# Kernel tuning notes

Hardware: AMD Instinct MI355X
Metric: run time of the kernel (lower is better)

Reference implementation:

```python
import jax, jax.numpy as jnp
import numpy as np

EPS = 1e-6

def safe_softmax(x, axis=-1):
    x_max = jnp.max(x, axis=axis, keepdims=True)
    x_exp = jnp.exp(x - x_max)
    return x_exp / (jnp.sum(x_exp, axis=axis, keepdims=True) + EPS)

def setup_inputs() -> dict:
    key = jax.random.key(0)
    ks = jax.random.split(key, 8)
    B, S, D = 16, 2048, 1024
    scale = 1.0 / np.sqrt(D)
    x = jax.random.normal(ks[0], (B, S, D), dtype=jnp.float32)
    y = jax.random.normal(ks[1], (B, S, D), dtype=jnp.float32)
    Wq = jax.random.normal(ks[2], (D, D), dtype=jnp.float32) * scale
    bq = jnp.zeros((D,), dtype=jnp.float32)
    Wk = jax.random.normal(ks[3], (D, D), dtype=jnp.float32) * scale
    bk = jnp.zeros((D,), dtype=jnp.float32)
    Wv = jax.random.normal(ks[4], (D, D), dtype=jnp.float32) * scale
    bv = jnp.zeros((D,), dtype=jnp.float32)
    return {"x": x, "y": y, "Wq": Wq, "bq": bq, "Wk": Wk, "bk": bk, "Wv": Wv, "bv": bv}

def reference(x, y, Wq, bq, Wk, bk, Wv, bv):
    # Q/K/V projections: [B, S, D]
    Q = jnp.einsum('bsd,df->bsf', x, Wq) + bq
    K = jnp.einsum('bsd,df->bsf', y, Wk) + bk
    V = jnp.einsum('bsd,df->bsf', y, Wv) + bv
    D = K.shape[-1]
    # single-head attention over full [B, Sq, Skv] score matrix
    logits = jnp.einsum('bqd,bkd->bqk', Q, K) / jnp.sqrt(jnp.float32(D))
    attn = safe_softmax(logits, axis=-1)
    out = jnp.einsum('bqk,bkd->bqd', attn, V)
    return out + x
```

## Files before the change

kernel.cpp:

```cpp
#include <hip/hip_runtime.h>
#include <hip/hip_bf16.h>

typedef __attribute__((ext_vector_type(8))) short bf16x8;
typedef __attribute__((ext_vector_type(4))) float f32x4;

__device__ __forceinline__ float bf2f(short u) {
  union { unsigned int u; float f; } c;
  c.u = ((unsigned int)(unsigned short)u) << 16;
  return c.f;
}
__device__ __forceinline__ short f2bf(float f) {
  union { float f; unsigned int u; } c; c.f = f;
  unsigned int r = (c.u + 0x7fffu + ((c.u >> 16) & 1u)) >> 16;
  return (short)(unsigned short)r;
}

__device__ __forceinline__ void gload16(const void* g, void* l) {
  __builtin_amdgcn_global_load_lds(
      (const __attribute__((address_space(1))) unsigned int*)g,
      (__attribute__((address_space(3))) unsigned int*)l, 16, 0, 0);
}

__global__ __launch_bounds__(256) void cvt_k(const float* __restrict__ in,
                                             short* __restrict__ out, int n4) {
  int i = blockIdx.x * blockDim.x + threadIdx.x;
  const int stride = gridDim.x * blockDim.x;
  for (; i < n4; i += stride) {
    float4 v = ((const float4*)in)[i];
    short4 o;
    o.x = f2bf(v.x); o.y = f2bf(v.y); o.z = f2bf(v.z); o.w = f2bf(v.w);
    ((short4*)out)[i] = o;
  }
}

__global__ __launch_bounds__(256) void cvtT_k(const float* __restrict__ W,
                                              short* __restrict__ Wt) {
  __shared__ float tile[32][33];
  const int n0 = blockIdx.x * 32, k0 = blockIdx.y * 32;
  const int tr = threadIdx.x >> 5;
  const int tc = threadIdx.x & 31;
#pragma unroll
  for (int p = 0; p < 4; ++p)
    tile[p * 8 + tr][tc] = W[(long long)(k0 + p * 8 + tr) * 1024 + n0 + tc];
  __syncthreads();
#pragma unroll
  for (int p = 0; p < 4; ++p)
    Wt[(long long)(n0 + p * 8 + tr) * 1024 + k0 + tc] = f2bf(tile[tc][p * 8 + tr]);
}


#define STG6(sp, ld8, dOff) do { \
  gload16((sp), Ls + (dOff)); \
  gload16((const char*)(sp) + (ld8), Ls + (dOff) + 512); } while (0)

#define RD_A6(BUF, QM) do { \
  _Pragma("unroll") \
  for (int mi = 0; mi < 4; ++mi) { \
    aR[mi][0] = *(const bf16x8*)(Ls + (BUF) + (QM)*8192 + arow + mi*1024 + aO0); \
    aR[mi][1] = *(const bf16x8*)(Ls + (BUF) + (QM)*8192 + arow + mi*1024 + aO1); \
  } } while (0)

#define RD_B6(DST, BUF, QN) do { \
  _Pragma("unroll") \
  for (int ni = 0; ni < 2; ++ni) { \
    DST[ni][0] = *(const bf16x8*)(Ls + (BUF) + 16384 + (QN)*8192 + brow + ni*1024 + aO0); \
    DST[ni][1] = *(const bf16x8*)(Ls + (BUF) + 16384 + (QN)*8192 + brow + ni*1024 + aO1); \
  } } while (0)

#define SYNCIN6 do { \
  __builtin_amdgcn_sched_barrier(0); \
  __builtin_amdgcn_s_barrier(); \
  asm volatile("s_waitcnt lgkmcnt(0)" ::: "memory"); \
  __builtin_amdgcn_sched_barrier(0); \
  __builtin_amdgcn_s_setprio(1); } while (0)

#define SYNCOUT6 do { \
  __builtin_amdgcn_s_setprio(0); \
  __builtin_amdgcn_s_barrier(); } while (0)

#define MF166(ACCQ, BB) do { \
  _Pragma("unroll") \
  for (int mi = 0; mi < 4; ++mi) { \
    _Pragma("unroll") \
    for (int ni = 0; ni < 2; ++ni) { \
      ACCQ[mi][ni] = __builtin_amdgcn_mfma_f32_16x16x32_bf16(aR[mi][0], BB[ni][0], ACCQ[mi][ni], 0, 0, 0); \
      ACCQ[mi][ni] = __builtin_amdgcn_mfma_f32_16x16x32_bf16(aR[mi][1], BB[ni][1], ACCQ[mi][ni], 0, 0, 0); \
    } \
  } } while (0)

template<int EPI>
__global__ __launch_bounds__(512) void gemm256_k(
    const short* __restrict__ A, const short* __restrict__ Bt,
    void* __restrict__ Cv, const float* __restrict__ X,
    int K, int lda, int ldb, int ldc) {
  __shared__ __align__(16) short Ls[65536];

  const int lane = threadIdx.x & 63;
  const int w = threadIdx.x >> 6;
  const int wm = w >> 2, wn = w & 3;
  const int w1k = w * 1024;
  const int l15 = lane & 15;
  const int g4 = lane >> 4;
  const int p8 = lane & 7;
  const int r8 = lane >> 3;
  const int aO0 = (g4 ^ p8) << 3;
  const int aO1 = ((4 + g4) ^ p8) << 3;
  const int arow = (wm * 64 + l15) * 64;
  const int brow = (wn * 32 + l15) * 64;

  const int gx = gridDim.x, gy = gridDim.y;
  const int nwg = gx * gy * gridDim.z;
  int lid = blockIdx.x + gx * (blockIdx.y + gy * blockIdx.z);
  lid = (lid & 7) * (nwg >> 3) + (lid >> 3);
  const int bx = lid % gx;
  const int rem = lid / gx;
  const int by = rem % gy;

  const int n0 = bx * 256;
  const int m0 = by * 256;
  const int nt = K >> 6;
  const int nit = nt >> 1;

  const long long ldaB = 2LL * lda, ldbB = 2LL * ldb;
  const long long ldaB8 = 8 * ldaB, ldbB8 = 8 * ldbB;
  const long long hOffA = 128 * ldaB, hOffB = 128 * ldbB;

  const char* pA = (const char*)A
      + (long long)(m0 + w * 16 + r8) * ldaB + ((p8 ^ r8) << 4);
  const char* pB = (const char*)Bt
      + (long long)(n0 + w * 16 + r8) * ldbB + ((p8 ^ r8) << 4);

  f32x4 acc[2][2][4][2] = {};
  bf16x8 aR[4][2], bR0[2][2], bR1[2][2];

  STG6(pA,                 ldaB8, 0 + w1k);
  STG6(pA + hOffA,         ldaB8, 8192 + w1k);
  STG6(pB,                 ldbB8, 16384 + w1k);
  STG6(pB + hOffB,         ldbB8, 24576 + w1k);
  STG6(pA + 128,           ldaB8, 32768 + w1k);
  STG6(pA + 128 + hOffA,   ldaB8, 40960 + w1k);
  STG6(pB + 128,           ldbB8, 49152 + w1k);
  STG6(pB + 128 + hOffB,   ldbB8, 57344 + w1k);
  asm volatile("s_waitcnt vmcnt(8)" ::: "memory");
  __builtin_amdgcn_s_barrier();

  for (int j = 0; j < nit; ++j) {
    const bool st = (j + 1 < nit);

    RD_A6(0, 0); RD_B6(bR0, 0, 0);
    SYNCIN6; MF166(acc[0][0], bR0); SYNCOUT6;
    RD_B6(bR1, 0, 1);
    if (st) { STG6(pA + 256, ldaB8, 0 + w1k);
              STG6(pB + 256, ldbB8, 16384 + w1k); }
    SYNCIN6; MF166(acc[0][1], bR1); SYNCOUT6;
    RD_A6(0, 1);
    if (st) STG6(pB + 256 + hOffB, ldbB8, 24576 + w1k);
    SYNCIN6; MF166(acc[1][1], bR1); SYNCOUT6;
    if (st) STG6(pA + 256 + hOffA, ldaB8, 8192 + w1k);
    SYNCIN6; MF166(acc[1][0], bR0);
    __builtin_amdgcn_s_setprio(0);
    if (st) asm volatile("s_waitcnt vmcnt(8)" ::: "memory");
    else    asm volatile("s_waitcnt vmcnt(0)" ::: "memory");
    __builtin_amdgcn_s_barrier();

    RD_A6(32768, 0); RD_B6(bR0, 32768, 0);
    SYNCIN6; MF166(acc[0][0], bR0); SYNCOUT6;
    RD_B6(bR1, 32768, 1);
    if (st) { STG6(pA + 384, ldaB8, 32768 + w1k);
              STG6(pB + 384, ldbB8, 49152 + w1k); }
    SYNCIN6; MF166(acc[0][1], bR1); SYNCOUT6;
    RD_A6(32768, 1);
    if (st) STG6(pB + 384 + hOffB, ldbB8, 57344 + w1k);
    SYNCIN6; MF166(acc[1][1], bR1); SYNCOUT6;
    if (st) STG6(pA + 384 + hOffA, ldaB8, 40960 + w1k);
    SYNCIN6; MF166(acc[1][0], bR0);
    __builtin_amdgcn_s_setprio(0);
    if (st) asm volatile("s_waitcnt vmcnt(8)" ::: "memory");
    __builtin_amdgcn_s_barrier();

    pA += 256; pB += 256;
  }

  const int rB = g4 * 4;
  if (EPI == 0) {
    short* C = (short*)Cv;
#pragma unroll
    for (int qn = 0; qn < 2; ++qn)
#pragma unroll
      for (int ni = 0; ni < 2; ++ni) {
        const int col = n0 + qn * 128 + wn * 32 + ni * 16 + l15;
        const float bv = X[col];
#pragma unroll
        for (int qm = 0; qm < 2; ++qm)
#pragma unroll
          for (int mi = 0; mi < 4; ++mi)
#pragma unroll
            for (int r = 0; r < 4; ++r) {
              const int row = m0 + qm * 128 + wm * 64 + mi * 16 + rB + r;
              C[(long long)row * ldc + col] = f2bf(acc[qm][qn][mi][ni][r] + bv);
            }
      }
  } else {
    short* C = (short*)Cv;
#pragma unroll
    for (int qn = 0; qn < 2; ++qn)
#pragma unroll
      for (int ni = 0; ni < 2; ++ni) {
        const int col = n0 + qn * 128 + wn * 32 + ni * 16 + l15;
        const int b2 = col >> 11;
        const int s = col & 2047;
#pragma unroll
        for (int qm = 0; qm < 2; ++qm)
#pragma unroll
          for (int mi = 0; mi < 4; ++mi)
#pragma unroll
            for (int r = 0; r < 4; ++r) {
              const int row = m0 + qm * 128 + wm * 64 + mi * 16 + rB + r;
              C[(long long)b2 * 2097152 + (long long)row * 2048 + s] =
                  f2bf(acc[qm][qn][mi][ni][r] + X[row]);
            }
      }
  }
}


template<int EPI>
__global__ __launch_bounds__(512, 4) void gemm8_k(
    const short* __restrict__ A, const short* __restrict__ Bt,
    void* __restrict__ Cv, const float* __restrict__ X,
    int K, int lda, int ldb, int ldc,
    long long strA, long long strB, long long strC, long long strX, float scale) {
  __shared__ __align__(16) short Ls[36864];

  const int lane = threadIdx.x & 63;
  const int w = threadIdx.x >> 6;
  const int wm = w >> 1, wn = w & 1;
  const int l15 = lane & 15;
  const int g4 = lane >> 4;
  const int swR = ((g4 ^ ((l15 >> 1) & 3)) << 3);
  const int arow = (wm * 64 + l15) * 32 + swR;
  const int brow = (wn * 64 + l15) * 32 + swR;
  const int sg = (lane & 3) ^ ((lane >> 3) & 3);

  const int gx = gridDim.x, gy = gridDim.y;
  const int nwg = gx * gy * gridDim.z;
  int lid = blockIdx.x + gx * (blockIdx.y + gy * blockIdx.z);
  lid = (lid & 7) * (nwg >> 3) + (lid >> 3);
  const int bx = lid % gx;
  const int rem = lid / gx;
  const int by = rem % gy;
  const int bz = rem / gy;

  const int n0 = bx * 128;
  const int m0 = by * 256;
  const int nt = K >> 5;

  const long long ldaB = 2LL * lda, ldbB = 2LL * ldb;
  const long long ldaB16 = 16 * ldaB;

  const char* pA = (const char*)(A + (long long)bz * strA)
      + (long long)(m0 + w * 32 + (lane >> 2)) * ldaB + sg * 16;
  const char* pB = (const char*)(Bt + (long long)bz * strB)
      + (long long)(n0 + w * 16 + (lane >> 2)) * ldbB + sg * 16;

  short* dA = Ls + w * 1024;
  short* dB = Ls + 8192 + w * 512;

  f32x4 acc[4][4] = {};

#pragma unroll
  for (int i = 0; i < 3; ++i) {
    const char* qA = pA + i * 64;
    gload16(qA,           dA + i * 12288);
    gload16(qA + ldaB16,  dA + i * 12288 + 512);
    gload16(pB + i * 64,  dB + i * 12288);
  }
  asm volatile("s_waitcnt vmcnt(6)" ::: "memory");
  __builtin_amdgcn_s_barrier();

  int cur = 0;
  for (int t = 0; t < nt; ++t) {
    const int bufO = cur * 12288;
    bf16x8 aR[4], bR[4];
#pragma unroll
    for (int mi = 0; mi < 4; ++mi)
      aR[mi] = *(const bf16x8*)(Ls + bufO + arow + mi * 512);
#pragma unroll
    for (int ni = 0; ni < 4; ++ni)
      bR[ni] = *(const bf16x8*)(Ls + bufO + 8192 + brow + ni * 512);
    asm volatile("s_waitcnt lgkmcnt(0)" ::: "memory");
    __builtin_amdgcn_s_barrier();
    if (t + 3 < nt) {
      const char* qA = pA + (t + 3) * 64;
      gload16(qA,          dA + bufO);
      gload16(qA + ldaB16, dA + bufO + 512);
      gload16(pB + (t + 3) * 64, dB + bufO);
    }
    __builtin_amdgcn_sched_barrier(0);
    __builtin_amdgcn_s_setprio(1);
#pragma unroll
    for (int mi = 0; mi < 4; ++mi)
#pragma unroll
      for (int ni = 0; ni < 4; ++ni)
        acc[mi][ni] = __builtin_amdgcn_mfma_f32_16x16x32_bf16(
            aR[mi], bR[ni], acc[mi][ni], 0, 0, 0);
    __builtin_amdgcn_s_setprio(0);
    if (t + 3 < nt)      asm volatile("s_waitcnt vmcnt(6)" ::: "memory");
    else if (t + 2 < nt) asm volatile("s_waitcnt vmcnt(3)" ::: "memory");
    else                 asm volatile("s_waitcnt vmcnt(0)" ::: "memory");
    __builtin_amdgcn_s_barrier();
    cur = (cur == 2) ? 0 : cur + 1;
  }

  const int rB = g4 * 4;
  if (EPI == 1) {
    short* C = (short*)Cv + (long long)bz * strC;
#pragma unroll
    for (int ni = 0; ni < 4; ++ni) {
      const int col = n0 + wn * 64 + ni * 16 + l15;
#pragma unroll
      for (int mi = 0; mi < 4; ++mi)
#pragma unroll
        for (int r = 0; r < 4; ++r) {
          const int row = m0 + wm * 64 + mi * 16 + rB + r;
          C[(long long)row * ldc + col] = f2bf(acc[mi][ni][r] * scale);
        }
    }
  } else {
    float* C = (float*)Cv + (long long)bz * strC;
    const float* Xb = X + (long long)bz * strX;
#pragma unroll
    for (int ni = 0; ni < 4; ++ni) {
      const int col = n0 + wn * 64 + ni * 16 + l15;
#pragma unroll
      for (int mi = 0; mi < 4; ++mi)
#pragma unroll
        for (int r = 0; r < 4; ++r) {
          const int row = m0 + wm * 64 + mi * 16 + rB + r;
          const long long idx = (long long)row * ldc + col;
          C[idx] = acc[mi][ni][r] + Xb[idx];
        }
    }
  }
}

__global__ __launch_bounds__(256) void softmax_k(short* __restrict__ P) {
  __shared__ float redm[4];
  __shared__ float reds[4];
  const long long row = blockIdx.x;
  short* p = P + row * 2048;
  const int t = threadIdx.x;
  const int w = t >> 6, lane = t & 63;
  bf16x8 v = *(const bf16x8*)(p + t * 8);
  float f[8];
  float mx = -3.0e38f;
#pragma unroll
  for (int j = 0; j < 8; ++j) { f[j] = bf2f(v[j]); mx = fmaxf(mx, f[j]); }
#pragma unroll
  for (int o = 32; o > 0; o >>= 1) mx = fmaxf(mx, __shfl_xor(mx, o));
  if (lane == 0) redm[w] = mx;
  __syncthreads();
  mx = fmaxf(fmaxf(redm[0], redm[1]), fmaxf(redm[2], redm[3]));
  float s = 0.f;
#pragma unroll
  for (int j = 0; j < 8; ++j) { f[j] = __expf(f[j] - mx); s += f[j]; }
#pragma unroll
  for (int o = 32; o > 0; o >>= 1) s += __shfl_xor(s, o);
  if (lane == 0) reds[w] = s;
  __syncthreads();
  s = reds[0] + reds[1] + reds[2] + reds[3];
  const float inv = 1.0f / (s + 1e-6f);
  bf16x8 o8;
#pragma unroll
  for (int j = 0; j < 8; ++j) o8[j] = f2bf(f[j] * inv);
  *(bf16x8*)(p + t * 8) = o8;
}

extern "C" void kernel_launch(void* const* d_in, const int* in_sizes, int n_in,
                              void* d_out, int out_size, void* d_ws, size_t ws_size,
                              hipStream_t stream) {
  const float* x  = (const float*)d_in[0];
  const float* y  = (const float*)d_in[1];
  const float* Wq = (const float*)d_in[2];
  const float* bq = (const float*)d_in[3];
  const float* Wk = (const float*)d_in[4];
  const float* bk = (const float*)d_in[5];
  const float* Wv = (const float*)d_in[6];
  const float* bv = (const float*)d_in[7];
  float* out = (float*)d_out;

  const long long SD  = 2048LL * 1024;
  const long long BSD = 16LL * SD;
  const long long SS  = 2048LL * 2048;

  char* ws = (char*)d_ws;
  short* xb  = (short*)ws;
  short* yb  = xb + BSD;
  short* Sl  = (short*)ws;
  short* Qb  = (short*)(ws + 134217728);
  short* Kb  = Qb + BSD;
  short* Vt  = Kb + BSD;
  short* Wqt = Vt + BSD;
  short* Wkt = Wqt + 1024 * 1024;
  short* Wvt = Wkt + 1024 * 1024;

  cvt_k<<<2048, 256, 0, stream>>>(x, xb, (int)(BSD / 4));
  cvt_k<<<2048, 256, 0, stream>>>(y, yb, (int)(BSD / 4));

  cvtT_k<<<dim3(32, 32), 256, 0, stream>>>(Wq, Wqt);
  cvtT_k<<<dim3(32, 32), 256, 0, stream>>>(Wk, Wkt);
  cvtT_k<<<dim3(32, 32), 256, 0, stream>>>(Wv, Wvt);

  gemm256_k<0><<<dim3(4, 128, 1), 512, 0, stream>>>(
      xb, Wqt, Qb, bq, 1024, 1024, 1024, 1024);
  gemm256_k<0><<<dim3(4, 128, 1), 512, 0, stream>>>(
      yb, Wkt, Kb, bk, 1024, 1024, 1024, 1024);
  gemm256_k<3><<<dim3(128, 4, 1), 512, 0, stream>>>(
      Wvt, yb, Vt, bv, 1024, 1024, 1024, 0);

  gemm8_k<1><<<dim3(16, 8, 16), 512, 0, stream>>>(
      Qb, Kb, Sl, nullptr, 1024, 1024, 1024, 2048, SD, SD, SS, 0, 0.03125f);

  softmax_k<<<32768, 256, 0, stream>>>(Sl);

  gemm8_k<2><<<dim3(8, 8, 16), 512, 0, stream>>>(
      Sl, Vt, out, x, 2048, 2048, 2048, 1024, SS, SD, SD, SD, 1.f);

  (void)in_sizes; (void)n_in; (void)out_size; (void)ws_size;
}
```

Before: 739.3 us.

## Compute P·V in FP8 with scaled softmax output and permuted K-layout

The softmax now writes probabilities scaled by 256 as FP8 into a separate buffer, and the V projection epilogue stores V^T as FP8. Both use a permuted position ordering so that each lane's 16-byte LDS read feeds two fp8 16x16x32 MFMAs. A new pv8_k kernel runs the P·V GEMM with fp8 MFMAs, then unscales and adds the residual. This halves the bytes moved for P and V and uses the faster fp8 MFMA rate, at the cost of lower precision in the attention weights and V.

```diff
diff --git a/kernel.cpp b/kernel.cpp
--- a/kernel.cpp
+++ b/kernel.cpp
@@ -3,6 +3,7 @@
 
 typedef __attribute__((ext_vector_type(8))) short bf16x8;
 typedef __attribute__((ext_vector_type(4))) float f32x4;
+typedef __attribute__((ext_vector_type(2))) long i64x2;
 
 __device__ __forceinline__ float bf2f(short u) {
   union { unsigned int u; float f; } c;
@@ -19,6 +20,10 @@
   __builtin_amdgcn_global_load_lds(
       (const __attribute__((address_space(1))) unsigned int*)g,
       (__attribute__((address_space(3))) unsigned int*)l, 16, 0, 0);
+}
+
+__device__ __forceinline__ int fp8_g(int s) {
+  return (s >> 6) * 64 + ((s >> 3) & 3) * 16 + ((s >> 5) & 1) * 8 + (s & 7);
 }
 
 __global__ __launch_bounds__(256) void cvt_k(const float* __restrict__ in,
@@ -201,7 +206,7 @@
             }
       }
   } else {
-    short* C = (short*)Cv;
+    unsigned char* C = (unsigned char*)Cv;
 #pragma unroll
     for (int qn = 0; qn < 2; ++qn)
 #pragma unroll
@@ -209,6 +214,7 @@
         const int col = n0 + qn * 128 + wn * 32 + ni * 16 + l15;
         const int b2 = col >> 11;
         const int s = col & 2047;
+        const int gs = fp8_g(s);
 #pragma unroll
         for (int qm = 0; qm < 2; ++qm)
 #pragma unroll
@@ -216,8 +222,10 @@
 #pragma unroll
             for (int r = 0; r < 4; ++r) {
               const int row = m0 + qm * 128 + wm * 64 + mi * 16 + rB + r;
-              C[(long long)b2 * 2097152 + (long long)row * 2048 + s] =
-                  f2bf(acc[qm][qn][mi][ni][r] + X[row]);
+              const float v = acc[qm][qn][mi][ni][r] + X[row];
+              const unsigned d = __builtin_amdgcn_cvt_pk_fp8_f32(v, v, 0, false);
+              C[(long long)b2 * 2097152 + (long long)row * 2048 + gs] =
+                  (unsigned char)(d & 0xff);
             }
       }
   }
@@ -313,42 +321,27 @@
   }
 
   const int rB = g4 * 4;
-  if (EPI == 1) {
-    short* C = (short*)Cv + (long long)bz * strC;
-#pragma unroll
-    for (int ni = 0; ni < 4; ++ni) {
-      const int col = n0 + wn * 64 + ni * 16 + l15;
-#pragma unroll
-      for (int mi = 0; mi < 4; ++mi)
-#pragma unroll
-        for (int r = 0; r < 4; ++r) {
-          const int row = m0 + wm * 64 + mi * 16 + rB + r;
-          C[(long long)row * ldc + col] = f2bf(acc[mi][ni][r] * scale);
-        }
-    }
-  } else {
-    float* C = (float*)Cv + (long long)bz * strC;
-    const float* Xb = X + (long long)bz * strX;
-#pragma unroll
-    for (int ni = 0; ni < 4; ++ni) {
-      const int col = n0 + wn * 64 + ni * 16 + l15;
-#pragma unroll
-      for (int mi = 0; mi < 4; ++mi)
-#pragma unroll
-        for (int r = 0; r < 4; ++r) {
-          const int row = m0 + wm * 64 + mi * 16 + rB + r;
-          const long long idx = (long long)row * ldc + col;
-          C[idx] = acc[mi][ni][r] + Xb[idx];
-        }
-    }
-  }
-}
-
-__global__ __launch_bounds__(256) void softmax_k(short* __restrict__ P) {
+  short* C = (short*)Cv + (long long)bz * strC;
+#pragma unroll
+  for (int ni = 0; ni < 4; ++ni) {
+    const int col = n0 + wn * 64 + ni * 16 + l15;
+#pragma unroll
+    for (int mi = 0; mi < 4; ++mi)
+#pragma unroll
+      for (int r = 0; r < 4; ++r) {
+        const int row = m0 + wm * 64 + mi * 16 + rB + r;
+        C[(long long)row * ldc + col] = f2bf(acc[mi][ni][r] * scale);
+      }
+  }
+  (void)X; (void)strX;
+}
+
+__global__ __launch_bounds__(256) void softmax8_k(const short* __restrict__ Sl,
+                                                  unsigned char* __restrict__ P8) {
   __shared__ float redm[4];
   __shared__ float reds[4];
   const long long row = blockIdx.x;
-  short* p = P + row * 2048;
+  const short* p = Sl + row * 2048;
   const int t = threadIdx.x;
   const int w = t >> 6, lane = t & 63;
   bf16x8 v = *(const bf16x8*)(p + t * 8);
@@ -369,11 +362,116 @@
   if (lane == 0) reds[w] = s;
   __syncthreads();
   s = reds[0] + reds[1] + reds[2] + reds[3];
-  const float inv = 1.0f / (s + 1e-6f);
-  bf16x8 o8;
-#pragma unroll
-  for (int j = 0; j < 8; ++j) o8[j] = f2bf(f[j] * inv);
-  *(bf16x8*)(p + t * 8) = o8;
+  const float inv = 256.0f / (s + 1e-6f);
+  unsigned d0 = __builtin_amdgcn_cvt_pk_fp8_f32(f[0] * inv, f[1] * inv, 0, false);
+  d0 = __builtin_amdgcn_cvt_pk_fp8_f32(f[2] * inv, f[3] * inv, d0, true);
+  unsigned d1 = __builtin_amdgcn_cvt_pk_fp8_f32(f[4] * inv, f[5] * inv, 0, false);
+  d1 = __builtin_amdgcn_cvt_pk_fp8_f32(f[6] * inv, f[7] * inv, d1, true);
+  const int grp = t >> 3, pc = t & 7;
+  unsigned char* dst = P8 + row * 2048 + grp * 64 + (pc & 3) * 16 + (pc >> 2) * 8;
+  *(unsigned long long*)dst =
+      (unsigned long long)d0 | ((unsigned long long)d1 << 32);
+}
+
+
+__global__ __launch_bounds__(512, 4) void pv8_k(
+    const unsigned char* __restrict__ P8, const unsigned char* __restrict__ V8,
+    float* __restrict__ Out, const float* __restrict__ x) {
+  __shared__ __align__(16) char Ls[73728];
+
+  const int lane = threadIdx.x & 63;
+  const int w = threadIdx.x >> 6;
+  const int wm = w >> 1, wn = w & 1;
+  const int l15 = lane & 15;
+  const int g4 = lane >> 4;
+  const int swB = ((g4 ^ ((l15 >> 1) & 3)) << 4);
+  const int arow = (wm * 64 + l15) * 64 + swB;
+  const int brow = (wn * 64 + l15) * 64 + swB;
+  const int sg = (lane & 3) ^ ((lane >> 3) & 3);
+
+  const int nwg = 1024;
+  int lid = blockIdx.x + 8 * (blockIdx.y + 8 * blockIdx.z);
+  lid = (lid & 7) * (nwg >> 3) + (lid >> 3);
+  const int bx = lid % 8;
+  const int rem = lid / 8;
+  const int by = rem % 8;
+  const int bz = rem / 8;
+  const int n0 = bx * 128, m0 = by * 256;
+  const int nt = 32;
+
+  const long long SD = 2097152LL;
+  const char* pA = (const char*)P8 + (long long)bz * 4194304LL
+      + (long long)(m0 + w * 32 + (lane >> 2)) * 2048 + sg * 16;
+  const char* pB = (const char*)V8 + (long long)bz * 2097152LL
+      + (long long)(n0 + w * 16 + (lane >> 2)) * 2048 + sg * 16;
+
+  char* dA = Ls + w * 2048;
+  char* dB = Ls + 16384 + w * 1024;
+
+  f32x4 acc[4][4] = {};
+
+#pragma unroll
+  for (int i = 0; i < 3; ++i) {
+    const char* qA = pA + i * 64;
+    gload16(qA,              dA + i * 24576);
+    gload16(qA + 16 * 2048,  dA + i * 24576 + 1024);
+    gload16(pB + i * 64,     dB + i * 24576);
+  }
+  asm volatile("s_waitcnt vmcnt(6)" ::: "memory");
+  __builtin_amdgcn_s_barrier();
+
+  int cur = 0;
+  for (int t = 0; t < nt; ++t) {
+    const int bufO = cur * 24576;
+    i64x2 aA[4], bB[4];
+#pragma unroll
+    for (int mi = 0; mi < 4; ++mi)
+      aA[mi] = *(const i64x2*)(Ls + bufO + arow + mi * 1024);
+#pragma unroll
+    for (int ni = 0; ni < 4; ++ni)
+      bB[ni] = *(const i64x2*)(Ls + bufO + 16384 + brow + ni * 1024);
+    asm volatile("s_waitcnt lgkmcnt(0)" ::: "memory");
+    __builtin_amdgcn_s_barrier();
+    if (t + 3 < nt) {
+      const char* qA = pA + (t + 3) * 64;
+      gload16(qA,             dA + bufO);
+      gload16(qA + 16 * 2048, dA + bufO + 1024);
+      gload16(pB + (t + 3) * 64, dB + bufO);
+    }
+    __builtin_amdgcn_sched_barrier(0);
+    __builtin_amdgcn_s_setprio(1);
+#pragma unroll
+    for (int mi = 0; mi < 4; ++mi)
+#pragma unroll
+      for (int ni = 0; ni < 4; ++ni) {
+        acc[mi][ni] = __builtin_amdgcn_mfma_f32_16x16x32_fp8_fp8(
+            aA[mi][0], bB[ni][0], acc[mi][ni], 0, 0, 0);
+        acc[mi][ni] = __builtin_amdgcn_mfma_f32_16x16x32_fp8_fp8(
+            aA[mi][1], bB[ni][1], acc[mi][ni], 0, 0, 0);
+      }
+    __builtin_amdgcn_s_setprio(0);
+    if (t + 3 < nt)      asm volatile("s_waitcnt vmcnt(6)" ::: "memory");
+    else if (t + 2 < nt) asm volatile("s_waitcnt vmcnt(3)" ::: "memory");
+    else                 asm volatile("s_waitcnt vmcnt(0)" ::: "memory");
+    __builtin_amdgcn_s_barrier();
+    cur = (cur == 2) ? 0 : cur + 1;
+  }
+
+  const int rB = g4 * 4;
+  float* C = Out + (long long)bz * SD;
+  const float* Xb = x + (long long)bz * SD;
+#pragma unroll
+  for (int ni = 0; ni < 4; ++ni) {
+    const int col = n0 + wn * 64 + ni * 16 + l15;
+#pragma unroll
+    for (int mi = 0; mi < 4; ++mi)
+#pragma unroll
+      for (int r = 0; r < 4; ++r) {
+        const int row = m0 + wm * 64 + mi * 16 + rB + r;
+        const long long idx = (long long)row * 1024 + col;
+        C[idx] = acc[mi][ni][r] * 0.00390625f + Xb[idx];
+      }
+  }
 }
 
 extern "C" void kernel_launch(void* const* d_in, const int* in_sizes, int n_in,
@@ -398,8 +496,10 @@
   short* yb  = xb + BSD;
   short* Sl  = (short*)ws;
   short* Qb  = (short*)(ws + 134217728);
+  unsigned char* P8 = (unsigned char*)Qb;
   short* Kb  = Qb + BSD;
   short* Vt  = Kb + BSD;
+  unsigned char* V8 = (unsigned char*)Vt;
   short* Wqt = Vt + BSD;
   short* Wkt = Wqt + 1024 * 1024;
   short* Wvt = Wkt + 1024 * 1024;
@@ -416,15 +516,14 @@
   gemm256_k<0><<<dim3(4, 128, 1), 512, 0, stream>>>(
       yb, Wkt, Kb, bk, 1024, 1024, 1024, 1024);
   gemm256_k<3><<<dim3(128, 4, 1), 512, 0, stream>>>(
-      Wvt, yb, Vt, bv, 1024, 1024, 1024, 0);
+      Wvt, yb, V8, bv, 1024, 1024, 1024, 0);
 
   gemm8_k<1><<<dim3(16, 8, 16), 512, 0, stream>>>(
       Qb, Kb, Sl, nullptr, 1024, 1024, 1024, 2048, SD, SD, SS, 0, 0.03125f);
 
-  softmax_k<<<32768, 256, 0, stream>>>(Sl);
-
-  gemm8_k<2><<<dim3(8, 8, 16), 512, 0, stream>>>(
-      Sl, Vt, out, x, 2048, 2048, 2048, 1024, SS, SD, SD, SD, 1.f);
+  softmax8_k<<<32768, 256, 0, stream>>>(Sl, P8);
+
+  pv8_k<<<dim3(8, 8, 16), 512, 0, stream>>>(P8, V8, out, x);
 
   (void)in_sizes; (void)n_in; (void)out_size; (void)ws_size;
 }
```

Result: faster. 676.8 us (-8.5%).

## Switch attention GEMMs to FP8 operands with permuted layout and scaled softmax output

Applied to the files above, without the earlier changes.

The Q/K/V projection epilogues now emit FP8 (e4m3) with a permuted column order that matches the FP8 MFMA operand layout. Softmax writes probabilities as FP8 scaled by 256, and both attention GEMMs use 16x16x32 fp8 MFMA with 64-byte K tiles and a doubled LDS buffer. The goal is to halve the bytes moved and raise matrix throughput, at the cost of lower precision in Q, K, V and P. The larger LDS footprint may also reduce occupancy.

```diff
diff --git a/kernel.cpp b/kernel.cpp
--- a/kernel.cpp
+++ b/kernel.cpp
@@ -3,6 +3,7 @@
 
 typedef __attribute__((ext_vector_type(8))) short bf16x8;
 typedef __attribute__((ext_vector_type(4))) float f32x4;
+typedef __attribute__((ext_vector_type(2))) long i64x2;
 
 __device__ __forceinline__ float bf2f(short u) {
   union { unsigned int u; float f; } c;
@@ -19,6 +20,10 @@
   __builtin_amdgcn_global_load_lds(
       (const __attribute__((address_space(1))) unsigned int*)g,
       (__attribute__((address_space(3))) unsigned int*)l, 16, 0, 0);
+}
+
+__device__ __forceinline__ int fp8_g(int s) {
+  return (s >> 6) * 64 + ((s >> 3) & 3) * 16 + ((s >> 5) & 1) * 8 + (s & 7);
 }
 
 __global__ __launch_bounds__(256) void cvt_k(const float* __restrict__ in,
@@ -182,26 +187,8 @@
   }
 
   const int rB = g4 * 4;
-  if (EPI == 0) {
-    short* C = (short*)Cv;
-#pragma unroll
-    for (int qn = 0; qn < 2; ++qn)
-#pragma unroll
-      for (int ni = 0; ni < 2; ++ni) {
-        const int col = n0 + qn * 128 + wn * 32 + ni * 16 + l15;
-        const float bv = X[col];
-#pragma unroll
-        for (int qm = 0; qm < 2; ++qm)
-#pragma unroll
-          for (int mi = 0; mi < 4; ++mi)
-#pragma unroll
-            for (int r = 0; r < 4; ++r) {
-              const int row = m0 + qm * 128 + wm * 64 + mi * 16 + rB + r;
-              C[(long long)row * ldc + col] = f2bf(acc[qm][qn][mi][ni][r] + bv);
-            }
-      }
-  } else {
-    short* C = (short*)Cv;
+  if (EPI == 3) {
+    unsigned char* C = (unsigned char*)Cv;
 #pragma unroll
     for (int qn = 0; qn < 2; ++qn)
 #pragma unroll
@@ -209,6 +196,7 @@
         const int col = n0 + qn * 128 + wn * 32 + ni * 16 + l15;
         const int b2 = col >> 11;
         const int s = col & 2047;
+        const int gs = fp8_g(s);
 #pragma unroll
         for (int qm = 0; qm < 2; ++qm)
 #pragma unroll
@@ -216,30 +204,90 @@
 #pragma unroll
             for (int r = 0; r < 4; ++r) {
               const int row = m0 + qm * 128 + wm * 64 + mi * 16 + rB + r;
-              C[(long long)b2 * 2097152 + (long long)row * 2048 + s] =
-                  f2bf(acc[qm][qn][mi][ni][r] + X[row]);
+              const float v = acc[qm][qn][mi][ni][r] + X[row];
+              const unsigned d = __builtin_amdgcn_cvt_pk_fp8_f32(v, v, 0, false);
+              C[(long long)b2 * 2097152 + (long long)row * 2048 + gs] =
+                  (unsigned char)(d & 0xff);
             }
       }
-  }
+  } else {
+    unsigned char* C = (unsigned char*)Cv;
+#pragma unroll
+    for (int qn = 0; qn < 2; ++qn)
+#pragma unroll
+      for (int ni = 0; ni < 2; ++ni) {
+        const int col = n0 + qn * 128 + wn * 32 + ni * 16 + l15;
+        const int gs = fp8_g(col);
+        const float bv = X[col];
+#pragma unroll
+        for (int qm = 0; qm < 2; ++qm)
+#pragma unroll
+          for (int mi = 0; mi < 4; ++mi)
+#pragma unroll
+            for (int r = 0; r < 4; ++r) {
+              const int row = m0 + qm * 128 + wm * 64 + mi * 16 + rB + r;
+              const float v = acc[qm][qn][mi][ni][r] + bv;
+              const unsigned d = __builtin_amdgcn_cvt_pk_fp8_f32(v, v, 0, false);
+              C[(long long)row * ldc + gs] = (unsigned char)(d & 0xff);
+            }
+      }
+  }
+}
+
+__global__ __launch_bounds__(256) void softmax8_k(const short* __restrict__ Sl,
+                                                  unsigned char* __restrict__ P8) {
+  __shared__ float redm[4];
+  __shared__ float reds[4];
+  const long long row = blockIdx.x;
+  const short* p = Sl + row * 2048;
+  const int t = threadIdx.x;
+  const int w = t >> 6, lane = t & 63;
+  bf16x8 v = *(const bf16x8*)(p + t * 8);
+  float f[8];
+  float mx = -3.0e38f;
+#pragma unroll
+  for (int j = 0; j < 8; ++j) { f[j] = bf2f(v[j]); mx = fmaxf(mx, f[j]); }
+#pragma unroll
+  for (int o = 32; o > 0; o >>= 1) mx = fmaxf(mx, __shfl_xor(mx, o));
+  if (lane == 0) redm[w] = mx;
+  __syncthreads();
+  mx = fmaxf(fmaxf(redm[0], redm[1]), fmaxf(redm[2], redm[3]));
+  float s = 0.f;
+#pragma unroll
+  for (int j = 0; j < 8; ++j) { f[j] = __expf(f[j] - mx); s += f[j]; }
+#pragma unroll
+  for (int o = 32; o > 0; o >>= 1) s += __shfl_xor(s, o);
+  if (lane == 0) reds[w] = s;
+  __syncthreads();
+  s = reds[0] + reds[1] + reds[2] + reds[3];
+  const float inv = 256.0f / (s + 1e-6f);
+  unsigned d0 = __builtin_amdgcn_cvt_pk_fp8_f32(f[0] * inv, f[1] * inv, 0, false);
+  d0 = __builtin_amdgcn_cvt_pk_fp8_f32(f[2] * inv, f[3] * inv, d0, true);
+  unsigned d1 = __builtin_amdgcn_cvt_pk_fp8_f32(f[4] * inv, f[5] * inv, 0, false);
+  d1 = __builtin_amdgcn_cvt_pk_fp8_f32(f[6] * inv, f[7] * inv, d1, true);
+  const int grp = t >> 3, pc = t & 7;
+  unsigned char* dst = P8 + row * 2048 + grp * 64 + (pc & 3) * 16 + (pc >> 2) * 8;
+  *(unsigned long long*)dst =
+      (unsigned long long)d0 | ((unsigned long long)d1 << 32);
 }
 
 
 template<int EPI>
-__global__ __launch_bounds__(512, 4) void gemm8_k(
-    const short* __restrict__ A, const short* __restrict__ Bt,
+__global__ __launch_bounds__(512, 4) void g8fp8_k(
+    const unsigned char* __restrict__ A8, const unsigned char* __restrict__ B8,
     void* __restrict__ Cv, const float* __restrict__ X,
-    int K, int lda, int ldb, int ldc,
+    int K, int ldaB, int ldbB, int ldc,
     long long strA, long long strB, long long strC, long long strX, float scale) {
-  __shared__ __align__(16) short Ls[36864];
+  __shared__ __align__(16) char Ls[73728];
 
   const int lane = threadIdx.x & 63;
   const int w = threadIdx.x >> 6;
   const int wm = w >> 1, wn = w & 1;
   const int l15 = lane & 15;
   const int g4 = lane >> 4;
-  const int swR = ((g4 ^ ((l15 >> 1) & 3)) << 3);
-  const int arow = (wm * 64 + l15) * 32 + swR;
-  const int brow = (wn * 64 + l15) * 32 + swR;
+  const int swB = ((g4 ^ ((l15 >> 1) & 3)) << 4);
+  const int arow = (wm * 64 + l15) * 64 + swB;
+  const int brow = (wn * 64 + l15) * 64 + swB;
   const int sg = (lane & 3) ^ ((lane >> 3) & 3);
 
   const int gx = gridDim.x, gy = gridDim.y;
@@ -250,50 +298,47 @@
   const int rem = lid / gx;
   const int by = rem % gy;
   const int bz = rem / gy;
-
-  const int n0 = bx * 128;
-  const int m0 = by * 256;
-  const int nt = K >> 5;
-
-  const long long ldaB = 2LL * lda, ldbB = 2LL * ldb;
-  const long long ldaB16 = 16 * ldaB;
-
-  const char* pA = (const char*)(A + (long long)bz * strA)
-      + (long long)(m0 + w * 32 + (lane >> 2)) * ldaB + sg * 16;
-  const char* pB = (const char*)(Bt + (long long)bz * strB)
-      + (long long)(n0 + w * 16 + (lane >> 2)) * ldbB + sg * 16;
-
-  short* dA = Ls + w * 1024;
-  short* dB = Ls + 8192 + w * 512;
+  const int n0 = bx * 128, m0 = by * 256;
+  const int nt = K >> 6;
+
+  const long long ldaL = ldaB, ldbL = ldbB;
+  const char* pA = (const char*)A8 + bz * strA
+      + (long long)(m0 + w * 32 + (lane >> 2)) * ldaL + sg * 16;
+  const char* pB = (const char*)B8 + bz * strB
+      + (long long)(n0 + w * 16 + (lane >> 2)) * ldbL + sg * 16;
+  const long long ldaL16 = 16 * ldaL;
+
+  char* dA = Ls + w * 2048;
+  char* dB = Ls + 16384 + w * 1024;
 
   f32x4 acc[4][4] = {};
 
 #pragma unroll
   for (int i = 0; i < 3; ++i) {
     const char* qA = pA + i * 64;
-    gload16(qA,           dA + i * 12288);
-    gload16(qA + ldaB16,  dA + i * 12288 + 512);
-    gload16(pB + i * 64,  dB + i * 12288);
+    gload16(qA,           dA + i * 24576);
+    gload16(qA + ldaL16,  dA + i * 24576 + 1024);
+    gload16(pB + i * 64,  dB + i * 24576);
   }
   asm volatile("s_waitcnt vmcnt(6)" ::: "memory");
   __builtin_amdgcn_s_barrier();
 
   int cur = 0;
   for (int t = 0; t < nt; ++t) {
-    const int bufO = cur * 12288;
-    bf16x8 aR[4], bR[4];
+    const int bufO = cur * 24576;
+    i64x2 aA[4], bB[4];
 #pragma unroll
     for (int mi = 0; mi < 4; ++mi)
-      aR[mi] = *(const bf16x8*)(Ls + bufO + arow + mi * 512);
+      aA[mi] = *(const i64x2*)(Ls + bufO + arow + mi * 1024);
 #pragma unroll
     for (int ni = 0; ni < 4; ++ni)
-      bR[ni] = *(const bf16x8*)(Ls + bufO + 8192 + brow + ni * 512);
+      bB[ni] = *(const i64x2*)(Ls + bufO + 16384 + brow + ni * 1024);
     asm volatile("s_waitcnt lgkmcnt(0)" ::: "memory");
     __builtin_amdgcn_s_barrier();
     if (t + 3 < nt) {
       const char* qA = pA + (t + 3) * 64;
       gload16(qA,          dA + bufO);
-      gload16(qA + ldaB16, dA + bufO + 512);
+      gload16(qA + ldaL16, dA + bufO + 1024);
       gload16(pB + (t + 3) * 64, dB + bufO);
     }
     __builtin_amdgcn_sched_barrier(0);
@@ -301,9 +346,12 @@
 #pragma unroll
     for (int mi = 0; mi < 4; ++mi)
 #pragma unroll
-      for (int ni = 0; ni < 4; ++ni)
-        acc[mi][ni] = __builtin_amdgcn_mfma_f32_16x16x32_bf16(
-            aR[mi], bR[ni], acc[mi][ni], 0, 0, 0);
+      for (int ni = 0; ni < 4; ++ni) {
+        acc[mi][ni] = __builtin_amdgcn_mfma_f32_16x16x32_fp8_fp8(
+            aA[mi][0], bB[ni][0], acc[mi][ni], 0, 0, 0);
+        acc[mi][ni] = __builtin_amdgcn_mfma_f32_16x16x32_fp8_fp8(
+            aA[mi][1], bB[ni][1], acc[mi][ni], 0, 0, 0);
+      }
     __builtin_amdgcn_s_setprio(0);
     if (t + 3 < nt)      asm volatile("s_waitcnt vmcnt(6)" ::: "memory");
     else if (t + 2 < nt) asm volatile("s_waitcnt vmcnt(3)" ::: "memory");
@@ -314,7 +362,7 @@
 
   const int rB = g4 * 4;
   if (EPI == 1) {
-    short* C = (short*)Cv + (long long)bz * strC;
+    short* C = (short*)Cv + bz * strC;
 #pragma unroll
     for (int ni = 0; ni < 4; ++ni) {
       const int col = n0 + wn * 64 + ni * 16 + l15;
@@ -327,8 +375,8 @@
         }
     }
   } else {
-    float* C = (float*)Cv + (long long)bz * strC;
-    const float* Xb = X + (long long)bz * strX;
+    float* C = (float*)Cv + bz * strC;
+    const float* Xb = X + bz * strX;
 #pragma unroll
     for (int ni = 0; ni < 4; ++ni) {
       const int col = n0 + wn * 64 + ni * 16 + l15;
@@ -338,42 +386,10 @@
         for (int r = 0; r < 4; ++r) {
           const int row = m0 + wm * 64 + mi * 16 + rB + r;
           const long long idx = (long long)row * ldc + col;
-          C[idx] = acc[mi][ni][r] + Xb[idx];
+          C[idx] = acc[mi][ni][r] * scale + Xb[idx];
         }
     }
   }
-}
-
-__global__ __launch_bounds__(256) void softmax_k(short* __restrict__ P) {
-  __shared__ float redm[4];
-  __shared__ float reds[4];
-  const long long row = blockIdx.x;
-  short* p = P + row * 2048;
-  const int t = threadIdx.x;
-  const int w = t >> 6, lane = t & 63;
-  bf16x8 v = *(const bf16x8*)(p + t * 8);
-  float f[8];
-  float mx = -3.0e38f;
-#pragma unroll
-  for (int j = 0; j < 8; ++j) { f[j] = bf2f(v[j]); mx = fmaxf(mx, f[j]); }
-#pragma unroll
-  for (int o = 32; o > 0; o >>= 1) mx = fmaxf(mx, __shfl_xor(mx, o));
-  if (lane == 0) redm[w] = mx;
-  __syncthreads();
-  mx = fmaxf(fmaxf(redm[0], redm[1]), fmaxf(redm[2], redm[3]));
-  float s = 0.f;
-#pragma unroll
-  for (int j = 0; j < 8; ++j) { f[j] = __expf(f[j] - mx); s += f[j]; }
-#pragma unroll
-  for (int o = 32; o > 0; o >>= 1) s += __shfl_xor(s, o);
-  if (lane == 0) reds[w] = s;
-  __syncthreads();
-  s = reds[0] + reds[1] + reds[2] + reds[3];
-  const float inv = 1.0f / (s + 1e-6f);
-  bf16x8 o8;
-#pragma unroll
-  for (int j = 0; j < 8; ++j) o8[j] = f2bf(f[j] * inv);
-  *(bf16x8*)(p + t * 8) = o8;
 }
 
 extern "C" void kernel_launch(void* const* d_in, const int* in_sizes, int n_in,
@@ -397,10 +413,11 @@
   short* xb  = (short*)ws;
   short* yb  = xb + BSD;
   short* Sl  = (short*)ws;
-  short* Qb  = (short*)(ws + 134217728);
-  short* Kb  = Qb + BSD;
-  short* Vt  = Kb + BSD;
-  short* Wqt = Vt + BSD;
+  unsigned char* Q8 = (unsigned char*)(ws + 134217728);
+  unsigned char* P8 = Q8;
+  unsigned char* K8 = (unsigned char*)(ws + 201326592);
+  unsigned char* V8 = (unsigned char*)(ws + 268435456);
+  short* Wqt = (short*)(ws + 335544320);
   short* Wkt = Wqt + 1024 * 1024;
   short* Wvt = Wkt + 1024 * 1024;
 
@@ -411,20 +428,22 @@
   cvtT_k<<<dim3(32, 32), 256, 0, stream>>>(Wk, Wkt);
   cvtT_k<<<dim3(32, 32), 256, 0, stream>>>(Wv, Wvt);
 
-  gemm256_k<0><<<dim3(4, 128, 1), 512, 0, stream>>>(
-      xb, Wqt, Qb, bq, 1024, 1024, 1024, 1024);
-  gemm256_k<0><<<dim3(4, 128, 1), 512, 0, stream>>>(
-      yb, Wkt, Kb, bk, 1024, 1024, 1024, 1024);
+  gemm256_k<4><<<dim3(4, 128, 1), 512, 0, stream>>>(
+      xb, Wqt, Q8, bq, 1024, 1024, 1024, 1024);
+  gemm256_k<4><<<dim3(4, 128, 1), 512, 0, stream>>>(
+      yb, Wkt, K8, bk, 1024, 1024, 1024, 1024);
   gemm256_k<3><<<dim3(128, 4, 1), 512, 0, stream>>>(
-      Wvt, yb, Vt, bv, 1024, 1024, 1024, 0);
-
-  gemm8_k<1><<<dim3(16, 8, 16), 512, 0, stream>>>(
-      Qb, Kb, Sl, nullptr, 1024, 1024, 1024, 2048, SD, SD, SS, 0, 0.03125f);
-
-  softmax_k<<<32768, 256, 0, stream>>>(Sl);
-
-  gemm8_k<2><<<dim3(8, 8, 16), 512, 0, stream>>>(
-      Sl, Vt, out, x, 2048, 2048, 2048, 1024, SS, SD, SD, SD, 1.f);
+      Wvt, yb, V8, bv, 1024, 1024, 1024, 0);
+
+  g8fp8_k<1><<<dim3(16, 8, 16), 512, 0, stream>>>(
+      Q8, K8, Sl, nullptr, 1024, 1024, 1024, 2048,
+      2097152LL, 2097152LL, SS, 0, 0.03125f);
+
+  softmax8_k<<<32768, 256, 0, stream>>>(Sl, P8);
+
+  g8fp8_k<2><<<dim3(8, 8, 16), 512, 0, stream>>>(
+      P8, V8, out, x, 2048, 2048, 2048, 1024,
+      4194304LL, 2097152LL, SD, SD, 0.00390625f);
 
   (void)in_sizes; (void)n_in; (void)out_size; (void)ws_size;
 }
```

After: 616.3 us. 16.6% less time.
